# Kernel tuning notes

Hardware: AMD Instinct MI355X
Metric: run time of the kernel (lower is better)

The kernel has to match this reference:

```python
import jax, jax.numpy as jnp
import numpy as np
from jax import lax

B, S, I, H = 256, 2048, 32, 18


def setup_inputs() -> dict:
    key = jax.random.key(0)
    ks = jax.random.split(key, 40)
    d = {}
    d['input'] = jax.random.normal(ks[0], (B, S, I), jnp.float32)
    d['hidden'] = jnp.zeros((3, B, H), jnp.float32)
    ki = 1
    sc = 1.0 / np.sqrt(H)
    for l in range(3):
        in_dim = I if l == 0 else H
        d[f'Wih{l}'] = jax.random.uniform(ks[ki], (H, in_dim), jnp.float32, -sc, sc); ki += 1
        d[f'bih{l}'] = jax.random.uniform(ks[ki], (H,), jnp.float32, -sc, sc); ki += 1
        d[f'Whh{l}'] = jax.random.uniform(ks[ki], (H, H), jnp.float32, -sc, sc); ki += 1
        d[f'bhh{l}'] = jax.random.uniform(ks[ki], (H,), jnp.float32, -sc, sc); ki += 1
    dims = [(H, H), (10, H), (8, 10), (4, 8), (2, 4), (1, 2)]
    for i, (o, ii) in enumerate(dims, start=1):
        s = 1.0 / np.sqrt(ii)
        d[f'W{i}'] = jax.random.uniform(ks[ki], (o, ii), jnp.float32, -s, s); ki += 1
        d[f'b{i}'] = jax.random.uniform(ks[ki], (o,), jnp.float32, -s, s); ki += 1
    return d


def _rnn_layer(x, h0, Wih, bih, Whh, bhh):
    # Precompute input contributions for all timesteps (one big GEMM),
    # then scan only the tiny hxh recurrence.
    xW = jnp.einsum('bsi,hi->bsh', x, Wih) + bih + bhh  # [B,S,H]

    def step(h, xw_t):
        h = jnp.tanh(xw_t + h @ Whh.T)
        return h, h

    hT, ys = lax.scan(step, h0, jnp.swapaxes(xW, 0, 1))  # scan over time
    return jnp.swapaxes(ys, 0, 1), hT


def reference(input, hidden,
              Wih0, bih0, Whh0, bhh0,
              Wih1, bih1, Whh1, bhh1,
              Wih2, bih2, Whh2, bhh2,
              W1, b1, W2, b2, W3, b3, W4, b4, W5, b5, W6, b6):
    layer_params = [(Wih0, bih0, Whh0, bhh0),
                    (Wih1, bih1, Whh1, bhh1),
                    (Wih2, bih2, Whh2, bhh2)]
    x = input
    h_finals = []
    for l, (Wih, bih, Whh, bhh) in enumerate(layer_params):
        x, hT = _rnn_layer(x, hidden[l], Wih, bih, Whh, bhh)
        h_finals.append(hT)
    hidden_out = jnp.stack(h_finals)  # [3,B,H]

    b_, s_, h_ = x.shape
    o = x.reshape(-1, h_)
    for W, b in [(W1, b1), (W2, b2), (W3, b3), (W4, b4), (W5, b5)]:
        o = jax.nn.relu(o @ W.T + b)
    o = o @ W6.T + b6
    return o.reshape(b_, s_, -1), hidden_out
```

## Files before the change

kernel.cpp:

```cpp
#include <hip/hip_runtime.h>

#define Bsz 256
#define Ssz 2048
#define Isz 32
#define Hsz 18
#define SCALE 2.885390081777927f

typedef float f2 __attribute__((ext_vector_type(2)));
typedef float f4 __attribute__((ext_vector_type(4)));

__device__ __forceinline__ float exp2_fast(float x) {
#if __has_builtin(__builtin_amdgcn_exp2f)
    return __builtin_amdgcn_exp2f(x);
#else
    return __expf(x * 0.6931471805599453f);
#endif
}

__global__ __launch_bounds__(256) void input_gemm(
    const float* __restrict__ x,
    const float* __restrict__ Wih0,
    const float* __restrict__ bih0,
    const float* __restrict__ bhh0,
    float* __restrict__ xw0T)
{
    __shared__ float xs[256 * 33];
    int blk = blockIdx.x;
    int b = blk >> 3;
    int t0 = (blk & 7) << 8;
    int tid = threadIdx.x;

    const float4* src = (const float4*)(x + ((size_t)b * Ssz + t0) * Isz);
#pragma unroll
    for (int k = 0; k < 8; ++k) {
        int l = k * 256 + tid;
        float4 v = src[l];
        int row = l >> 3, k4 = l & 7;
        float* p = xs + row * 33 + k4 * 4;
        p[0] = v.x; p[1] = v.y; p[2] = v.z; p[3] = v.w;
    }
    __syncthreads();

    float xv[32];
    const float* myrow = xs + tid * 33;
#pragma unroll
    for (int k = 0; k < 32; ++k) xv[k] = myrow[k];

    float* op = xw0T + (size_t)b * (Hsz * Ssz) + (t0 + tid);
#pragma unroll
    for (int ii = 0; ii < Hsz; ++ii) {
        float acc = bih0[ii] + bhh0[ii];
#pragma unroll
        for (int k = 0; k < 32; ++k) acc = fmaf(xv[k], Wih0[ii * Isz + k], acc);
        op[(size_t)ii * Ssz] = acc * SCALE;
    }
}

__global__ __launch_bounds__(64) void rnn_scan(
    const float* __restrict__ xw0T,
    const float* __restrict__ hidden,
    const float* __restrict__ Whh0,
    const float* __restrict__ Wih1, const float* __restrict__ bih1,
    const float* __restrict__ Whh1, const float* __restrict__ bhh1,
    const float* __restrict__ Wih2, const float* __restrict__ bih2,
    const float* __restrict__ Whh2, const float* __restrict__ bhh2,
    float* __restrict__ h2T,
    float* __restrict__ hid_out)
{
    const int b = blockIdx.x;
    const int r = threadIdx.x;
    const int g = (r < 18) ? 0 : (r < 36) ? 1 : (r < 54) ? 2 : 3;
    const int i = r - g * 18;
    const bool lane_active = (g < 3);
    const bool g0lane = (g == 0);
    const bool g2lane = (g == 2);

    __shared__ __align__(16) float X[96];
    for (int k = r; k < 96; k += 64) X[k] = 0.0f;
    __builtin_amdgcn_wave_barrier();

    float w[36];
    float econst = 0.0f;
    float h = 0.0f;
    if (lane_active) {
        const float* Whh = (g == 0) ? Whh0 : (g == 1) ? Whh1 : Whh2;
#pragma unroll
        for (int j = 0; j < Hsz; ++j) w[18 + j] = Whh[i * Hsz + j] * SCALE;
        if (g >= 1) {
            const float* Wih = (g == 1) ? Wih1 : Wih2;
            const float* bi  = (g == 1) ? bih1 : bih2;
            const float* bh  = (g == 1) ? bhh1 : bhh2;
#pragma unroll
            for (int j = 0; j < Hsz; ++j) w[j] = Wih[i * Hsz + j] * SCALE;
            econst = (bi[i] + bh[i]) * SCALE;
        } else {
#pragma unroll
            for (int j = 0; j < Hsz; ++j) w[j] = 0.0f;
        }
        h = hidden[(g * Bsz + b) * Hsz + i];
    } else {
#pragma unroll
        for (int j = 0; j < 36; ++j) w[j] = 0.0f;
    }

    f2 w2[18];
#pragma unroll
    for (int k = 0; k < 18; ++k) w2[k] = f2{w[2 * k], w[2 * k + 1]};

    const int ws = 18 + r;
    const f2* xw2r = (const f2*)(X + 18 * g);

    X[ws] = h;
    __builtin_amdgcn_wave_barrier();

    const float* xwp = xw0T + (size_t)b * (Hsz * Ssz) + (size_t)((g == 0) ? i : 0) * Ssz;
    float*       hop2 = h2T + (size_t)b * (Hsz * Ssz) + (size_t)i * Ssz;

    f4 cur = *(const f4*)(xwp + 0);
    f4 nxt = *(const f4*)(xwp + 4);
    f4 ob;

    auto do_tick = [&](float e, bool dostore, int st) -> float {
        f2 d0  = xw2r[0],  d1  = xw2r[1],  d2  = xw2r[2],  d3  = xw2r[3];
        f2 d4  = xw2r[4],  d5  = xw2r[5],  d6  = xw2r[6],  d7  = xw2r[7];
        f2 d8  = xw2r[8],  d9  = xw2r[9],  d10 = xw2r[10], d11 = xw2r[11];
        f2 d12 = xw2r[12], d13 = xw2r[13], d14 = xw2r[14], d15 = xw2r[15];
        f2 d16 = xw2r[16], d17 = xw2r[17];
        if (dostore && g2lane) *(f4*)(hop2 + st) = ob;
        f2 a0 = f2{e, 0.0f}, a1 = f2{0.0f, 0.0f}, a2 = f2{0.0f, 0.0f};
        a0 = __builtin_elementwise_fma(w2[0],  d0,  a0);
        a1 = __builtin_elementwise_fma(w2[1],  d1,  a1);
        a2 = __builtin_elementwise_fma(w2[2],  d2,  a2);
        a0 = __builtin_elementwise_fma(w2[3],  d3,  a0);
        a1 = __builtin_elementwise_fma(w2[4],  d4,  a1);
        a2 = __builtin_elementwise_fma(w2[5],  d5,  a2);
        a0 = __builtin_elementwise_fma(w2[6],  d6,  a0);
        a1 = __builtin_elementwise_fma(w2[7],  d7,  a1);
        a2 = __builtin_elementwise_fma(w2[8],  d8,  a2);
        a0 = __builtin_elementwise_fma(w2[9],  d9,  a0);
        a1 = __builtin_elementwise_fma(w2[10], d10, a1);
        a2 = __builtin_elementwise_fma(w2[11], d11, a2);
        a0 = __builtin_elementwise_fma(w2[12], d12, a0);
        a1 = __builtin_elementwise_fma(w2[13], d13, a1);
        a2 = __builtin_elementwise_fma(w2[14], d14, a2);
        a0 = __builtin_elementwise_fma(w2[15], d15, a0);
        a1 = __builtin_elementwise_fma(w2[16], d16, a1);
        a2 = __builtin_elementwise_fma(w2[17], d17, a2);
        f2 s = (a0 + a1) + a2;
        float a = s.x + s.y;
        float t = exp2_fast(a);
        return fmaf(-2.0f, __builtin_amdgcn_rcpf(t + 1.0f), 1.0f);
    };

    {
        f4 fut = *(const f4*)(xwp + 8);
        float ev[4] = {cur.x, cur.y, cur.z, cur.w};
#pragma unroll
        for (int u = 0; u < 4; ++u) {
            const int T = u;
            float e = g0lane ? ev[u] : econst;
            float nh = do_tick(e, false, 0);
            bool upd = lane_active && (T >= g);
            h = upd ? nh : h;
            X[ws] = h;
            if (u == 2) ob.x = h; else if (u == 3) ob.y = h;
            __builtin_amdgcn_wave_barrier();
        }
        cur = nxt; nxt = fut;
    }

    for (int tb = 4; tb < Ssz; tb += 4) {
        int tl = tb + 8; if (tl > Ssz - 4) tl = Ssz - 4;
        f4 fut = *(const f4*)(xwp + tl);
        float ev[4] = {cur.x, cur.y, cur.z, cur.w};
#pragma unroll
        for (int u = 0; u < 4; ++u) {
            float e = g0lane ? ev[u] : econst;
            h = do_tick(e, u == 2, tb - 4);
            X[ws] = h;
            if (u == 0) ob.z = h;
            else if (u == 1) ob.w = h;
            else if (u == 2) ob.x = h;
            else ob.y = h;
            __builtin_amdgcn_wave_barrier();
        }
        cur = nxt; nxt = fut;
    }

    {
        float ev[2] = {cur.x, cur.y};
#pragma unroll
        for (int u = 0; u < 2; ++u) {
            const int T = Ssz + u;
            float e = g0lane ? ev[u] : econst;
            float nh = do_tick(e, false, 0);
            bool upd = lane_active && (T <= Ssz - 1 + g);
            h = upd ? nh : h;
            X[ws] = h;
            if (u == 0) ob.z = h; else ob.w = h;
            __builtin_amdgcn_wave_barrier();
        }
        if (g2lane) *(f4*)(hop2 + Ssz - 4) = ob;
    }

    if (lane_active) hid_out[(g * Bsz + b) * Hsz + i] = h;
}

__global__ __launch_bounds__(256) void mlp_head(
    const float* __restrict__ h2T,
    const float* __restrict__ W1, const float* __restrict__ b1,
    const float* __restrict__ W2, const float* __restrict__ b2,
    const float* __restrict__ W3, const float* __restrict__ b3,
    const float* __restrict__ W4, const float* __restrict__ b4,
    const float* __restrict__ W5, const float* __restrict__ b5,
    const float* __restrict__ W6, const float* __restrict__ b6,
    float* __restrict__ out)
{
    int idx = blockIdx.x * 256 + threadIdx.x;
    int b = idx >> 11;
    int t = idx & (Ssz - 1);
    const float* hp = h2T + (size_t)b * (Hsz * Ssz) + t;
    float v[Hsz];
#pragma unroll
    for (int j = 0; j < Hsz; ++j) v[j] = hp[(size_t)j * Ssz];

    float a1[18];
#pragma unroll
    for (int o = 0; o < 18; ++o) {
        float acc = b1[o];
#pragma unroll
        for (int j = 0; j < 18; ++j) acc = fmaf(W1[o * 18 + j], v[j], acc);
        a1[o] = fmaxf(acc, 0.0f);
    }
    float a2[10];
#pragma unroll
    for (int o = 0; o < 10; ++o) {
        float acc = b2[o];
#pragma unroll
        for (int j = 0; j < 18; ++j) acc = fmaf(W2[o * 18 + j], a1[j], acc);
        a2[o] = fmaxf(acc, 0.0f);
    }
    float a3[8];
#pragma unroll
    for (int o = 0; o < 8; ++o) {
        float acc = b3[o];
#pragma unroll
        for (int j = 0; j < 10; ++j) acc = fmaf(W3[o * 10 + j], a2[j], acc);
        a3[o] = fmaxf(acc, 0.0f);
    }
    float a4[4];
#pragma unroll
    for (int o = 0; o < 4; ++o) {
        float acc = b4[o];
#pragma unroll
        for (int j = 0; j < 8; ++j) acc = fmaf(W4[o * 8 + j], a3[j], acc);
        a4[o] = fmaxf(acc, 0.0f);
    }
    float a5[2];
#pragma unroll
    for (int o = 0; o < 2; ++o) {
        float acc = b5[o];
#pragma unroll
        for (int j = 0; j < 4; ++j) acc = fmaf(W5[o * 4 + j], a4[j], acc);
        a5[o] = fmaxf(acc, 0.0f);
    }
    float r6 = b6[0];
    r6 = fmaf(W6[0], a5[0], r6);
    r6 = fmaf(W6[1], a5[1], r6);
    out[idx] = r6;
}

extern "C" void kernel_launch(void* const* d_in, const int* in_sizes, int n_in,
                              void* d_out, int out_size, void* d_ws, size_t ws_size,
                              hipStream_t stream) {
    (void)in_sizes; (void)n_in; (void)out_size; (void)ws_size;
    const float* input  = (const float*)d_in[0];
    const float* hidden = (const float*)d_in[1];
    const float* Wih0 = (const float*)d_in[2];  const float* bih0 = (const float*)d_in[3];
    const float* Whh0 = (const float*)d_in[4];  const float* bhh0 = (const float*)d_in[5];
    const float* Wih1 = (const float*)d_in[6];  const float* bih1 = (const float*)d_in[7];
    const float* Whh1 = (const float*)d_in[8];  const float* bhh1 = (const float*)d_in[9];
    const float* Wih2 = (const float*)d_in[10]; const float* bih2 = (const float*)d_in[11];
    const float* Whh2 = (const float*)d_in[12]; const float* bhh2 = (const float*)d_in[13];
    const float* W1 = (const float*)d_in[14]; const float* b1 = (const float*)d_in[15];
    const float* W2 = (const float*)d_in[16]; const float* b2 = (const float*)d_in[17];
    const float* W3 = (const float*)d_in[18]; const float* b3 = (const float*)d_in[19];
    const float* W4 = (const float*)d_in[20]; const float* b4 = (const float*)d_in[21];
    const float* W5 = (const float*)d_in[22]; const float* b5 = (const float*)d_in[23];
    const float* W6 = (const float*)d_in[24]; const float* b6 = (const float*)d_in[25];

    float* xw0T = (float*)d_ws;
    float* h2T  = xw0T + (size_t)Bsz * Hsz * Ssz;
    float* out  = (float*)d_out;
    float* hout = out + (size_t)Bsz * Ssz;

    input_gemm<<<dim3(2048), dim3(256), 0, stream>>>(input, Wih0, bih0, bhh0, xw0T);
    rnn_scan<<<dim3(256), dim3(64), 0, stream>>>(xw0T, hidden, Whh0,
                                                 Wih1, bih1, Whh1, bhh1,
                                                 Wih2, bih2, Whh2, bhh2,
                                                 h2T, hout);
    mlp_head<<<dim3(2048), dim3(256), 0, stream>>>(h2T, W1, b1, W2, b2, W3, b3,
                                                   W4, b4, W5, b5, W6, b6, out);
}
```

Baseline: 470.6 us.

## Split recurrence into input and hidden halves to shorten per-tick critical path

Restructures the wavefront-skewed 3-layer RNN recurrence so each tick computes the hidden-hidden dot product on the critical path. The input-projection half for the next step is computed after h is written, overlapping with the barrier. Layer skew grows from one to two ticks per layer, the LDS layout is padded to 20-float stride for f4 reads, and the output-store schedule shifts to match. The aim is lower serial latency per timestep at the cost of extra pipeline ticks and more subtle indexing that could break correctness.

```diff
diff --git a/kernel.cpp b/kernel.cpp
--- a/kernel.cpp
+++ b/kernel.cpp
@@ -8,6 +8,9 @@
 
 typedef float f2 __attribute__((ext_vector_type(2)));
 typedef float f4 __attribute__((ext_vector_type(4)));
+
+#define LO2(v) __builtin_shufflevector(v, v, 0, 1)
+#define HI2(v) __builtin_shufflevector(v, v, 2, 3)
 
 __device__ __forceinline__ float exp2_fast(float x) {
 #if __has_builtin(__builtin_amdgcn_exp2f)
@@ -75,8 +78,8 @@
     const bool g0lane = (g == 0);
     const bool g2lane = (g == 2);
 
-    __shared__ __align__(16) float X[96];
-    for (int k = r; k < 96; k += 64) X[k] = 0.0f;
+    __shared__ __align__(16) float X[112];
+    for (int k = r; k < 112; k += 64) X[k] = 0.0f;
     __builtin_amdgcn_wave_barrier();
 
     float w[36];
@@ -103,12 +106,21 @@
         for (int j = 0; j < 36; ++j) w[j] = 0.0f;
     }
 
-    f2 w2[18];
-#pragma unroll
-    for (int k = 0; k < 18; ++k) w2[k] = f2{w[2 * k], w[2 * k + 1]};
-
-    const int ws = 18 + r;
-    const f2* xw2r = (const f2*)(X + 18 * g);
+    f4 wx4[4], wh4[4];
+    f2 wxt, wht;
+#pragma unroll
+    for (int k = 0; k < 4; ++k) {
+        wx4[k] = f4{w[4*k], w[4*k+1], w[4*k+2], w[4*k+3]};
+        wh4[k] = f4{w[18+4*k], w[18+4*k+1], w[18+4*k+2], w[18+4*k+3]};
+    }
+    wxt = f2{w[16], w[17]};
+    wht = f2{w[34], w[35]};
+
+    const int ws = 20 * (g + 1) + i;
+    const f4* ro4 = (const f4*)(X + 20 * (g + 1));
+    const f2* ro2 = (const f2*)(X + 20 * (g + 1) + 16);
+    const f4* rx4 = (const f4*)(X + 20 * g);
+    const f2* rx2 = (const f2*)(X + 20 * g + 16);
 
     X[ws] = h;
     __builtin_amdgcn_wave_barrier();
@@ -119,52 +131,58 @@
     f4 cur = *(const f4*)(xwp + 0);
     f4 nxt = *(const f4*)(xwp + 4);
     f4 ob;
-
-    auto do_tick = [&](float e, bool dostore, int st) -> float {
-        f2 d0  = xw2r[0],  d1  = xw2r[1],  d2  = xw2r[2],  d3  = xw2r[3];
-        f2 d4  = xw2r[4],  d5  = xw2r[5],  d6  = xw2r[6],  d7  = xw2r[7];
-        f2 d8  = xw2r[8],  d9  = xw2r[9],  d10 = xw2r[10], d11 = xw2r[11];
-        f2 d12 = xw2r[12], d13 = xw2r[13], d14 = xw2r[14], d15 = xw2r[15];
-        f2 d16 = xw2r[16], d17 = xw2r[17];
+    f2 xp;
+
+    {
+        f4 x0 = rx4[0], x1 = rx4[1], x2 = rx4[2], x3 = rx4[3];
+        f2 x4 = rx2[0];
+        float e0 = g0lane ? cur.x : econst;
+        f4 p0 = __builtin_elementwise_fma(wx4[0], x0, f4{e0, 0.0f, 0.0f, 0.0f});
+        f4 p1 = __builtin_elementwise_fma(wx4[1], x1, f4{0.0f, 0.0f, 0.0f, 0.0f});
+        p0 = __builtin_elementwise_fma(wx4[2], x2, p0);
+        p1 = __builtin_elementwise_fma(wx4[3], x3, p1);
+        f2 pt = __builtin_elementwise_fma(wxt, x4, f2{0.0f, 0.0f});
+        f4 q = p0 + p1;
+        xp = (LO2(q) + HI2(q)) + pt;
+    }
+
+    auto tick = [&](float e_next, bool use_mask, bool upd, bool dostore, int st) {
+        f4 o0 = ro4[0], o1 = ro4[1], o2 = ro4[2], o3 = ro4[3];
+        f2 o4 = ro2[0];
+        f4 x0 = rx4[0], x1 = rx4[1], x2 = rx4[2], x3 = rx4[3];
+        f2 x4 = rx2[0];
         if (dostore && g2lane) *(f4*)(hop2 + st) = ob;
-        f2 a0 = f2{e, 0.0f}, a1 = f2{0.0f, 0.0f}, a2 = f2{0.0f, 0.0f};
-        a0 = __builtin_elementwise_fma(w2[0],  d0,  a0);
-        a1 = __builtin_elementwise_fma(w2[1],  d1,  a1);
-        a2 = __builtin_elementwise_fma(w2[2],  d2,  a2);
-        a0 = __builtin_elementwise_fma(w2[3],  d3,  a0);
-        a1 = __builtin_elementwise_fma(w2[4],  d4,  a1);
-        a2 = __builtin_elementwise_fma(w2[5],  d5,  a2);
-        a0 = __builtin_elementwise_fma(w2[6],  d6,  a0);
-        a1 = __builtin_elementwise_fma(w2[7],  d7,  a1);
-        a2 = __builtin_elementwise_fma(w2[8],  d8,  a2);
-        a0 = __builtin_elementwise_fma(w2[9],  d9,  a0);
-        a1 = __builtin_elementwise_fma(w2[10], d10, a1);
-        a2 = __builtin_elementwise_fma(w2[11], d11, a2);
-        a0 = __builtin_elementwise_fma(w2[12], d12, a0);
-        a1 = __builtin_elementwise_fma(w2[13], d13, a1);
-        a2 = __builtin_elementwise_fma(w2[14], d14, a2);
-        a0 = __builtin_elementwise_fma(w2[15], d15, a0);
-        a1 = __builtin_elementwise_fma(w2[16], d16, a1);
-        a2 = __builtin_elementwise_fma(w2[17], d17, a2);
-        f2 s = (a0 + a1) + a2;
-        float a = s.x + s.y;
+        f4 a0 = __builtin_elementwise_fma(wh4[0], o0, f4{0.0f, 0.0f, 0.0f, 0.0f});
+        f4 a1 = __builtin_elementwise_fma(wh4[1], o1, f4{0.0f, 0.0f, 0.0f, 0.0f});
+        a0 = __builtin_elementwise_fma(wh4[2], o2, a0);
+        a1 = __builtin_elementwise_fma(wh4[3], o3, a1);
+        f2 at = __builtin_elementwise_fma(wht, o4, xp);
+        f4 s4 = a0 + a1;
+        f2 s2 = (LO2(s4) + HI2(s4)) + at;
+        float a = s2.x + s2.y;
         float t = exp2_fast(a);
-        return fmaf(-2.0f, __builtin_amdgcn_rcpf(t + 1.0f), 1.0f);
+        float nh = fmaf(-2.0f, __builtin_amdgcn_rcpf(t + 1.0f), 1.0f);
+        h = use_mask ? (upd ? nh : h) : nh;
+        X[ws] = h;
+        f4 p0 = __builtin_elementwise_fma(wx4[0], x0, f4{e_next, 0.0f, 0.0f, 0.0f});
+        f4 p1 = __builtin_elementwise_fma(wx4[1], x1, f4{0.0f, 0.0f, 0.0f, 0.0f});
+        p0 = __builtin_elementwise_fma(wx4[2], x2, p0);
+        p1 = __builtin_elementwise_fma(wx4[3], x3, p1);
+        f2 pt = __builtin_elementwise_fma(wxt, x4, f2{0.0f, 0.0f});
+        f4 q = p0 + p1;
+        xp = (LO2(q) + HI2(q)) + pt;
+        __builtin_amdgcn_wave_barrier();
     };
 
     {
         f4 fut = *(const f4*)(xwp + 8);
-        float ev[4] = {cur.x, cur.y, cur.z, cur.w};
+        float en[4] = {cur.y, cur.z, cur.w, nxt.x};
 #pragma unroll
         for (int u = 0; u < 4; ++u) {
             const int T = u;
-            float e = g0lane ? ev[u] : econst;
-            float nh = do_tick(e, false, 0);
-            bool upd = lane_active && (T >= g);
-            h = upd ? nh : h;
-            X[ws] = h;
-            if (u == 2) ob.x = h; else if (u == 3) ob.y = h;
-            __builtin_amdgcn_wave_barrier();
+            float e_next = g0lane ? en[u] : econst;
+            bool upd = lane_active && (T >= 2 * g);
+            tick(e_next, true, upd, false, 0);
         }
         cur = nxt; nxt = fut;
     }
@@ -172,33 +190,31 @@
     for (int tb = 4; tb < Ssz; tb += 4) {
         int tl = tb + 8; if (tl > Ssz - 4) tl = Ssz - 4;
         f4 fut = *(const f4*)(xwp + tl);
-        float ev[4] = {cur.x, cur.y, cur.z, cur.w};
+        float en[4] = {cur.y, cur.z, cur.w, nxt.x};
 #pragma unroll
         for (int u = 0; u < 4; ++u) {
-            float e = g0lane ? ev[u] : econst;
-            h = do_tick(e, u == 2, tb - 4);
-            X[ws] = h;
-            if (u == 0) ob.z = h;
-            else if (u == 1) ob.w = h;
-            else if (u == 2) ob.x = h;
-            else ob.y = h;
-            __builtin_amdgcn_wave_barrier();
+            float e_next = g0lane ? en[u] : econst;
+            tick(e_next, false, false, (u == 0) && (tb >= 8), tb - 8);
+            if (u == 0) ob.x = h;
+            else if (u == 1) ob.y = h;
+            else if (u == 2) ob.z = h;
+            else ob.w = h;
         }
         cur = nxt; nxt = fut;
     }
 
     {
-        float ev[2] = {cur.x, cur.y};
-#pragma unroll
-        for (int u = 0; u < 2; ++u) {
+        float en[4] = {cur.y, cur.z, cur.w, cur.w};
+#pragma unroll
+        for (int u = 0; u < 4; ++u) {
             const int T = Ssz + u;
-            float e = g0lane ? ev[u] : econst;
-            float nh = do_tick(e, false, 0);
-            bool upd = lane_active && (T <= Ssz - 1 + g);
-            h = upd ? nh : h;
-            X[ws] = h;
-            if (u == 0) ob.z = h; else ob.w = h;
-            __builtin_amdgcn_wave_barrier();
+            float e_next = g0lane ? en[u] : econst;
+            bool upd = lane_active && (T <= Ssz - 1 + 2 * g);
+            tick(e_next, true, upd, (u == 0), Ssz - 8);
+            if (u == 0) ob.x = h;
+            else if (u == 1) ob.y = h;
+            else if (u == 2) ob.z = h;
+            else ob.w = h;
         }
         if (g2lane) *(f4*)(hop2 + Ssz - 4) = ob;
     }
```

New measurement: 458.0 us. 2.7% less time.
